# Optimization experiments

Measured on AMD Instinct MI355X. Metric: run time of the kernel, lower is better.

## Reference

```python
import jax, jax.numpy as jnp
import numpy as np

B, L, N, H = 512, 50, 16, 128
NUM_USERS = NUM_ITEMS = 100000


def setup_inputs() -> dict:
    key = jax.random.key(0)
    ks = jax.random.split(key, 20)
    s = lambda i, shape: jax.random.normal(ks[i], shape, dtype=jnp.float32) * 0.05
    return {
        "user_ids": jax.random.randint(ks[0], (B,), 0, NUM_USERS),
        "item_ids": jax.random.randint(ks[1], (B,), 0, NUM_ITEMS),
        "history": jax.random.randint(ks[2], (B, L), 0, NUM_ITEMS),
        "neighbor_emb": jax.random.normal(ks[3], (B, L, N, H), dtype=jnp.float32),
        "user_table": s(4, (NUM_USERS, H)),
        "item_table": s(5, (NUM_ITEMS, H)),
        "Wa": s(6, (2 * H, 96)), "ba": jnp.zeros((96,), jnp.float32),
        "W1": s(7, (96, 48)), "b1": jnp.zeros((48,), jnp.float32),
        "W2": s(8, (48, 16)), "b2": jnp.zeros((16,), jnp.float32),
        "W3": s(9, (16, 1)), "b3": jnp.zeros((1,), jnp.float32),
        # 4 heads of Linear(H, H//4) concatenated on the output dim == one [H, H] GEMM
        "Wmh": s(10, (H, H)), "bmh": jnp.zeros((H,), jnp.float32),
        "Wfc1": s(11, (2 * H, H)), "bfc1": jnp.zeros((H,), jnp.float32),
        "Wout": s(12, (H, 1)), "bout": jnp.zeros((1,), jnp.float32),
    }


def reference(user_ids, item_ids, history, neighbor_emb,
              user_table, item_table, Wa, ba, W1, b1, W2, b2, W3, b3,
              Wmh, bmh, Wfc1, bfc1, Wout, bout):
    user_emb = user_table[user_ids]                      # [B, H]
    item_emb = item_table[item_ids]                      # computed but unused (as in original)
    hist_emb = item_table[history]                       # [B, L, H]

    # concat(history broadcast over neighbors, neighbor_emb) -> [B, L, N, 2H]
    hist_b = jnp.broadcast_to(hist_emb[:, :, None, :], (B, L, N, H))
    att_in = jnp.concatenate([hist_b, neighbor_emb], axis=-1)

    scores = jax.nn.relu(att_in @ Wa + ba)               # [B, L, N, 96]
    h1 = jax.nn.relu(scores @ W1 + b1)                   # [B, L, N, 48]
    h2 = jax.nn.relu(h1 @ W2 + b2)                       # [B, L, N, 16]
    logits = (h2 @ W3 + b3)[..., 0]                      # [B, L, N]
    attn = jax.nn.softmax(logits, axis=-1)               # softmax over neighbor dim

    agg = jnp.einsum('bln,blnh->blh', attn, neighbor_emb)  # [B, L, H]
    mh = agg @ Wmh + bmh                                 # fused multihead projections
    pooled = mh.mean(axis=1)                             # [B, H]

    comb = jnp.concatenate([user_emb, pooled], axis=-1)  # [B, 2H]
    hidden = jax.nn.relu(comb @ Wfc1 + bfc1)             # dropout is identity in eval
    out = jax.nn.sigmoid(hidden @ Wout + bout)[:, 0]     # [B]
    return out
```

## Files before the change

### kernel.cpp

```cpp
#include <hip/hip_runtime.h>

constexpr int B  = 512, L = 50, N = 16, H = 128;
constexpr int C1 = 96, C2 = 48, C3 = 16;

typedef __bf16   bf16x8 __attribute__((ext_vector_type(8)));
typedef float    f32x4  __attribute__((ext_vector_type(4)));
typedef unsigned u32x4  __attribute__((ext_vector_type(4)));

__device__ __forceinline__ bf16x8 cvt8(float4 a, float4 b) {
  bf16x8 r;
  r[0] = (__bf16)a.x; r[1] = (__bf16)a.y; r[2] = (__bf16)a.z; r[3] = (__bf16)a.w;
  r[4] = (__bf16)b.x; r[5] = (__bf16)b.y; r[6] = (__bf16)b.z; r[7] = (__bf16)b.w;
  return r;
}
__device__ __forceinline__ float bf16lo(unsigned u) { return __uint_as_float(u << 16); }
__device__ __forceinline__ float bf16hi(unsigned u) { return __uint_as_float(u & 0xffff0000u); }
__device__ __forceinline__ unsigned pkbf(float lo, float hi) {
  unsigned r;
  asm("v_cvt_pk_bf16_f32 %0, %1, %2" : "=v"(r) : "v"(lo), "v"(hi));
  return r;
}

__global__ __launch_bounds__(256, 2) void fused_kernel(
    const int*   __restrict__ user_ids,
    const int*   __restrict__ history,
    const float* __restrict__ neighbor_emb,
    const float* __restrict__ user_table,
    const float* __restrict__ item_table,
    const float* __restrict__ Wa,  const float* __restrict__ ba,
    const float* __restrict__ W1,  const float* __restrict__ b1,
    const float* __restrict__ W2,  const float* __restrict__ b2,
    const float* __restrict__ W3,
    const float* __restrict__ Wmh,  const float* __restrict__ bmh,
    const float* __restrict__ Wfc1, const float* __restrict__ bfc1,
    const float* __restrict__ Wout, const float* __restrict__ bout,
    float* __restrict__ out)
{
  __shared__ __align__(16) __bf16 sWa[48 * 64 * 8];
  __shared__ __align__(16) __bf16 sW1[9 * 64 * 8];
  __shared__ __align__(16) __bf16 sW2f[2 * 64 * 8];
  __shared__ __align__(16) __bf16 sHS[4][16 * C1];
  __shared__ __align__(16) float sB1[48];
  __shared__ __align__(16) float sB2[16];
  __shared__ __align__(16) float sW3v[16];
  __shared__ float sRed[4][128];
  __shared__ float sAgg2[128];
  __shared__ float sComb[2 * H];
  __shared__ float sP[4];

  const int tid  = threadIdx.x;
  const int wave = tid >> 6;
  const int lane = tid & 63;
  const int g    = lane >> 4;
  const int c    = lane & 15;

  for (int e = tid; e < 48 * 64; e += 256) {
    int lv = e & 63, frag = e >> 6;
    int s = frag & 7, t = frag >> 3;
    int k0 = s * 32 + ((lv >> 4) << 3);
    int cc = t * 16 + (lv & 15);
    bf16x8 v;
    #pragma unroll
    for (int j = 0; j < 8; ++j) v[j] = (__bf16)Wa[(k0 + j) * C1 + cc];
    *(bf16x8*)&sWa[e * 8] = v;
  }
  for (int e = tid; e < 9 * 64; e += 256) {
    int lv = e & 63, frag = e >> 6;
    int s = frag % 3, t = frag / 3;
    int k0 = s * 32 + ((lv >> 4) << 3);
    int cc = t * 16 + (lv & 15);
    bf16x8 v;
    #pragma unroll
    for (int j = 0; j < 8; ++j) v[j] = (__bf16)W1[(k0 + j) * C2 + cc];
    *(bf16x8*)&sW1[e * 8] = v;
  }
  for (int e = tid; e < 2 * 64; e += 256) {
    int lv = e & 63, s = e >> 6;
    bf16x8 v;
    #pragma unroll
    for (int j = 0; j < 8; ++j) {
      int k = s * 32 + ((lv >> 4) << 3) + j;
      v[j] = (k < C2) ? (__bf16)W2[k * C3 + (lv & 15)] : (__bf16)0.f;
    }
    *(bf16x8*)&sW2f[e * 8] = v;
  }
  if (tid < 48) sB1[tid] = b1[tid];
  if (tid < 16) { sB2[tid] = b2[tid]; sW3v[tid] = W3[tid]; }

  __syncthreads();

  const int bb = blockIdx.x;
  const int wl = wave;
  __bf16* HS = sHS[wave];
  const int nIter = (L - wl + 3) / 4;

  {
    float ba_r[6];
    #pragma unroll
    for (int t = 0; t < 6; ++t) ba_r[t] = ba[t * 16 + c];
    int li  = wl + 4 * c;
    int idx = (li < L) ? history[bb * L + li] : history[bb * L];
    const float* hr = item_table + (size_t)idx * H;
    f32x4 acch[6];
    #pragma unroll
    for (int t = 0; t < 6; ++t) acch[t] = (f32x4){0.f, 0.f, 0.f, 0.f};
    #pragma unroll
    for (int s = 0; s < 4; ++s) {
      const float* p = hr + s * 32 + g * 8;
      bf16x8 a = cvt8(*(const float4*)p, *(const float4*)(p + 4));
      #pragma unroll
      for (int t = 0; t < 6; ++t)
        acch[t] = __builtin_amdgcn_mfma_f32_16x16x32_bf16(
            a, *(const bf16x8*)&sWa[((t * 8 + s) * 64 + lane) * 8], acch[t], 0, 0, 0);
    }
    #pragma unroll
    for (int t = 0; t < 6; ++t)
      #pragma unroll
      for (int r = 0; r < 4; ++r)
        HS[(4 * g + r) * C1 + t * 16 + c] = (__bf16)(acch[t][r] + ba_r[t]);
  }

  const float* nb0 = neighbor_emb + (size_t)(bb * L + wl) * (N * H) + c * H + g * 8;
  const size_t TS = (size_t)4 * N * H;
  float4 nf[8];
  #pragma unroll
  for (int s = 0; s < 4; ++s) {
    nf[2 * s]     = *(const float4*)(nb0 + s * 32);
    nf[2 * s + 1] = *(const float4*)(nb0 + s * 32 + 4);
  }
  float aggp[32];
  #pragma unroll
  for (int i = 0; i < 32; ++i) aggp[i] = 0.f;

  const int  src_lo = ((g & 1) << 5) | c;
  const int  src_hi = src_lo + 16;
  const bool gh     = (g >> 1) & 1;

  for (int it = 0; it < nIter; ++it) {
    bf16x8 aA[4];
    #pragma unroll
    for (int s = 0; s < 4; ++s) aA[s] = cvt8(nf[2 * s], nf[2 * s + 1]);
    if (it + 1 < nIter) {
      const float* p = nb0 + (size_t)(it + 1) * TS;
      #pragma unroll
      for (int s = 0; s < 4; ++s) {
        nf[2 * s]     = *(const float4*)(p + s * 32);
        nf[2 * s + 1] = *(const float4*)(p + s * 32 + 4);
      }
    }

    unsigned lo_ = 0;
    asm volatile("" : "+v"(lo_));
    const f32x4 b1v0 = *(const f32x4*)&sB1[ 0 + 4 * g + lo_];
    const f32x4 b1v1 = *(const f32x4*)&sB1[16 + 4 * g + lo_];
    const f32x4 b1v2 = *(const f32x4*)&sB1[32 + 4 * g + lo_];
    const f32x4 b2v  = *(const f32x4*)&sB2[4 * g + lo_];
    const f32x4 w3v  = *(const f32x4*)&sW3v[4 * g + lo_];
    const bf16x8 w2f0 = *(const bf16x8*)&sW2f[(0 * 64 + lane) * 8 + lo_ * 8];
    const bf16x8 w2f1 = *(const bf16x8*)&sW2f[(1 * 64 + lane) * 8 + lo_ * 8];

    f32x4 acc[6];
    #pragma unroll
    for (int t = 0; t < 6; ++t) {
      uint2 hw = *(const uint2*)&HS[it * C1 + 16 * t + 4 * g];
      acc[t][0] = bf16lo(hw.x); acc[t][1] = bf16hi(hw.x);
      acc[t][2] = bf16lo(hw.y); acc[t][3] = bf16hi(hw.y);
    }
    #pragma unroll
    for (int s = 0; s < 4; ++s)
      #pragma unroll
      for (int t = 0; t < 6; ++t)
        acc[t] = __builtin_amdgcn_mfma_f32_16x16x32_bf16(
            *(const bf16x8*)&sWa[((t * 8 + 4 + s) * 64 + lane) * 8], aA[s],
            acc[t], 0, 0, 0);
    unsigned pku[6][2];
    #pragma unroll
    for (int t = 0; t < 6; ++t) {
      pku[t][0] = pkbf(fmaxf(acc[t][0], 0.f), fmaxf(acc[t][1], 0.f));
      pku[t][1] = pkbf(fmaxf(acc[t][2], 0.f), fmaxf(acc[t][3], 0.f));
    }

    f32x4 acc2[3] = {b1v0, b1v1, b1v2};
    #pragma unroll
    for (int s = 0; s < 3; ++s) {
      unsigned a0 = __shfl((int)pku[2 * s][0], src_lo);
      unsigned a1 = __shfl((int)pku[2 * s][1], src_lo);
      unsigned a2 = __shfl((int)pku[2 * s][0], src_hi);
      unsigned a3 = __shfl((int)pku[2 * s][1], src_hi);
      unsigned d0 = __shfl((int)pku[2 * s + 1][0], src_lo);
      unsigned d1 = __shfl((int)pku[2 * s + 1][1], src_lo);
      unsigned d2 = __shfl((int)pku[2 * s + 1][0], src_hi);
      unsigned d3 = __shfl((int)pku[2 * s + 1][1], src_hi);
      u32x4 wv = {gh ? d0 : a0, gh ? d1 : a1, gh ? d2 : a2, gh ? d3 : a3};
      bf16x8 bf2 = __builtin_bit_cast(bf16x8, wv);
      #pragma unroll
      for (int t2 = 0; t2 < 3; ++t2)
        acc2[t2] = __builtin_amdgcn_mfma_f32_16x16x32_bf16(
            *(const bf16x8*)&sW1[((t2 * 3 + s) * 64 + lane) * 8], bf2,
            acc2[t2], 0, 0, 0);
    }
    unsigned pk2[3][2];
    #pragma unroll
    for (int t2 = 0; t2 < 3; ++t2) {
      pk2[t2][0] = pkbf(fmaxf(acc2[t2][0], 0.f), fmaxf(acc2[t2][1], 0.f));
      pk2[t2][1] = pkbf(fmaxf(acc2[t2][2], 0.f), fmaxf(acc2[t2][3], 0.f));
    }

    f32x4 acc3 = b2v;
    {
      unsigned a0 = __shfl((int)pk2[0][0], src_lo);
      unsigned a1 = __shfl((int)pk2[0][1], src_lo);
      unsigned a2 = __shfl((int)pk2[0][0], src_hi);
      unsigned a3 = __shfl((int)pk2[0][1], src_hi);
      unsigned d0 = __shfl((int)pk2[1][0], src_lo);
      unsigned d1 = __shfl((int)pk2[1][1], src_lo);
      unsigned d2 = __shfl((int)pk2[1][0], src_hi);
      unsigned d3 = __shfl((int)pk2[1][1], src_hi);
      u32x4 wv = {gh ? d0 : a0, gh ? d1 : a1, gh ? d2 : a2, gh ? d3 : a3};
      acc3 = __builtin_amdgcn_mfma_f32_16x16x32_bf16(
          w2f0, __builtin_bit_cast(bf16x8, wv), acc3, 0, 0, 0);
      unsigned e0 = __shfl((int)pk2[2][0], src_lo);
      unsigned e1 = __shfl((int)pk2[2][1], src_lo);
      unsigned e2 = __shfl((int)pk2[2][0], src_hi);
      unsigned e3 = __shfl((int)pk2[2][1], src_hi);
      u32x4 wv2 = {gh ? 0u : e0, gh ? 0u : e1, gh ? 0u : e2, gh ? 0u : e3};
      acc3 = __builtin_amdgcn_mfma_f32_16x16x32_bf16(
          w2f1, __builtin_bit_cast(bf16x8, wv2), acc3, 0, 0, 0);
    }

    float lg = 0.f;
    #pragma unroll
    for (int r = 0; r < 4; ++r) lg = fmaf(fmaxf(acc3[r], 0.f), w3v[r], lg);
    lg += __shfl_xor(lg, 16);
    lg += __shfl_xor(lg, 32);
    float e = __expf(lg);
    float se = e;
    se += __shfl_xor(se, 1);
    se += __shfl_xor(se, 2);
    se += __shfl_xor(se, 4);
    se += __shfl_xor(se, 8);
    const float w = e / se;

    #pragma unroll
    for (int s = 0; s < 4; ++s) {
      u32x4 au = __builtin_bit_cast(u32x4, aA[s]);
      #pragma unroll
      for (int q = 0; q < 4; ++q) {
        unsigned u = au[q];
        aggp[s * 8 + 2 * q]     = fmaf(w, bf16lo(u), aggp[s * 8 + 2 * q]);
        aggp[s * 8 + 2 * q + 1] = fmaf(w, bf16hi(u), aggp[s * 8 + 2 * q + 1]);
      }
    }
  }

  #pragma unroll
  for (int off = 1; off < 16; off <<= 1)
    #pragma unroll
    for (int i = 0; i < 32; ++i) aggp[i] += __shfl_xor(aggp[i], off);
  if (c == 0) {
    #pragma unroll
    for (int s = 0; s < 4; ++s) {
      float4 v0 = {aggp[8 * s + 0], aggp[8 * s + 1], aggp[8 * s + 2], aggp[8 * s + 3]};
      float4 v1 = {aggp[8 * s + 4], aggp[8 * s + 5], aggp[8 * s + 6], aggp[8 * s + 7]};
      *(float4*)&sRed[wave][32 * s + 8 * g]     = v0;
      *(float4*)&sRed[wave][32 * s + 8 * g + 4] = v1;
    }
  }
  __syncthreads();

  if (tid < 128) {
    float s = 0.f;
    #pragma unroll
    for (int w = 0; w < 4; ++w) s += sRed[w][tid];
    sAgg2[tid] = s * (1.0f / L);
    sComb[tid] = user_table[(size_t)user_ids[bb] * H + tid];
  }
  __syncthreads();
  if (tid < 128) {
    float p = bmh[tid];
    #pragma unroll 8
    for (int k = 0; k < H; ++k) p = fmaf(sAgg2[k], Wmh[k * H + tid], p);
    sComb[H + tid] = p;
  }
  __syncthreads();
  if (tid < 128) {
    float hd = bfc1[tid];
    #pragma unroll 8
    for (int k = 0; k < 2 * H; ++k) hd = fmaf(sComb[k], Wfc1[k * H + tid], hd);
    hd = fmaxf(hd, 0.f);
    float partial = hd * Wout[tid];
    #pragma unroll
    for (int off = 32; off > 0; off >>= 1) partial += __shfl_down(partial, off);
    if (lane == 0) sP[wave] = partial;
  }
  __syncthreads();
  if (tid == 0)
    out[bb] = 1.f / (1.f + __expf(-(sP[0] + sP[1] + bout[0])));
}

extern "C" void kernel_launch(void* const* d_in, const int* in_sizes, int n_in,
                              void* d_out, int out_size, void* d_ws, size_t ws_size,
                              hipStream_t stream) {
  const int*   user_ids     = (const int*)  d_in[0];
  const int*   history      = (const int*)  d_in[2];
  const float* neighbor_emb = (const float*)d_in[3];
  const float* user_table   = (const float*)d_in[4];
  const float* item_table   = (const float*)d_in[5];
  const float* Wa   = (const float*)d_in[6];
  const float* ba   = (const float*)d_in[7];
  const float* W1   = (const float*)d_in[8];
  const float* b1   = (const float*)d_in[9];
  const float* W2   = (const float*)d_in[10];
  const float* b2   = (const float*)d_in[11];
  const float* W3   = (const float*)d_in[12];
  const float* Wmh  = (const float*)d_in[14];
  const float* bmh  = (const float*)d_in[15];
  const float* Wfc1 = (const float*)d_in[16];
  const float* bfc1 = (const float*)d_in[17];
  const float* Wout = (const float*)d_in[18];
  const float* bout = (const float*)d_in[19];

  float* out = (float*)d_out;

  hipLaunchKernelGGL(fused_kernel, dim3(B), dim3(256), 0, stream,
                     user_ids, history, neighbor_emb, user_table, item_table,
                     Wa, ba, W1, b1, W2, b2, W3,
                     Wmh, bmh, Wfc1, bfc1, Wout, bout, out);
}
```

Baseline: 59.52 us.

## Split attention across two blocks per batch row and move MLP head to separate kernel

The fused kernel is split in two. The attention kernel now launches two blocks per batch row, each handling half the history positions, and writes partial aggregates to workspace. A second small kernel combines the halves and runs the Wmh/Wfc1/output head. Wa is staged in LDS one half at a time (history half, then neighbor half) to cut shared memory, which may allow higher occupancy. The cost is an extra launch, a workspace round trip, and Wa being re-staged once per block.

```diff
diff --git a/kernel.cpp b/kernel.cpp
--- a/kernel.cpp
+++ b/kernel.cpp
@@ -21,32 +21,24 @@
   return r;
 }
 
-__global__ __launch_bounds__(256, 2) void fused_kernel(
-    const int*   __restrict__ user_ids,
+__global__ __launch_bounds__(256, 2) void attn_kernel(
     const int*   __restrict__ history,
     const float* __restrict__ neighbor_emb,
-    const float* __restrict__ user_table,
     const float* __restrict__ item_table,
     const float* __restrict__ Wa,  const float* __restrict__ ba,
     const float* __restrict__ W1,  const float* __restrict__ b1,
     const float* __restrict__ W2,  const float* __restrict__ b2,
     const float* __restrict__ W3,
-    const float* __restrict__ Wmh,  const float* __restrict__ bmh,
-    const float* __restrict__ Wfc1, const float* __restrict__ bfc1,
-    const float* __restrict__ Wout, const float* __restrict__ bout,
-    float* __restrict__ out)
+    float* __restrict__ ws)
 {
-  __shared__ __align__(16) __bf16 sWa[48 * 64 * 8];
+  __shared__ __align__(16) __bf16 sWa[24 * 64 * 8];
   __shared__ __align__(16) __bf16 sW1[9 * 64 * 8];
   __shared__ __align__(16) __bf16 sW2f[2 * 64 * 8];
-  __shared__ __align__(16) __bf16 sHS[4][16 * C1];
+  __shared__ __align__(16) __bf16 sHS[4][8 * C1];
   __shared__ __align__(16) float sB1[48];
   __shared__ __align__(16) float sB2[16];
   __shared__ __align__(16) float sW3v[16];
   __shared__ float sRed[4][128];
-  __shared__ float sAgg2[128];
-  __shared__ float sComb[2 * H];
-  __shared__ float sP[4];
 
   const int tid  = threadIdx.x;
   const int wave = tid >> 6;
@@ -54,9 +46,13 @@
   const int g    = lane >> 4;
   const int c    = lane & 15;
 
-  for (int e = tid; e < 48 * 64; e += 256) {
+  const int bb     = blockIdx.x >> 1;
+  const int half   = blockIdx.x & 1;
+  const int stream = half * 4 + wave;
+
+  for (int e = tid; e < 24 * 64; e += 256) {
     int lv = e & 63, frag = e >> 6;
-    int s = frag & 7, t = frag >> 3;
+    int s = frag & 3, t = frag >> 2;
     int k0 = s * 32 + ((lv >> 4) << 3);
     int cc = t * 16 + (lv & 15);
     bf16x8 v;
@@ -89,16 +85,14 @@
 
   __syncthreads();
 
-  const int bb = blockIdx.x;
-  const int wl = wave;
   __bf16* HS = sHS[wave];
-  const int nIter = (L - wl + 3) / 4;
+  const int nIter = (L - stream + 7) / 8;
 
   {
     float ba_r[6];
     #pragma unroll
     for (int t = 0; t < 6; ++t) ba_r[t] = ba[t * 16 + c];
-    int li  = wl + 4 * c;
+    int li  = stream + 8 * c;
     int idx = (li < L) ? history[bb * L + li] : history[bb * L];
     const float* hr = item_table + (size_t)idx * H;
     f32x4 acch[6];
@@ -111,17 +105,33 @@
       #pragma unroll
       for (int t = 0; t < 6; ++t)
         acch[t] = __builtin_amdgcn_mfma_f32_16x16x32_bf16(
-            a, *(const bf16x8*)&sWa[((t * 8 + s) * 64 + lane) * 8], acch[t], 0, 0, 0);
-    }
-    #pragma unroll
-    for (int t = 0; t < 6; ++t)
-      #pragma unroll
-      for (int r = 0; r < 4; ++r)
-        HS[(4 * g + r) * C1 + t * 16 + c] = (__bf16)(acch[t][r] + ba_r[t]);
-  }
-
-  const float* nb0 = neighbor_emb + (size_t)(bb * L + wl) * (N * H) + c * H + g * 8;
-  const size_t TS = (size_t)4 * N * H;
+            a, *(const bf16x8*)&sWa[((t * 4 + s) * 64 + lane) * 8], acch[t], 0, 0, 0);
+    }
+    if (g < 2) {
+      #pragma unroll
+      for (int t = 0; t < 6; ++t)
+        #pragma unroll
+        for (int r = 0; r < 4; ++r)
+          HS[(4 * g + r) * C1 + t * 16 + c] = (__bf16)(acch[t][r] + ba_r[t]);
+    }
+  }
+
+  __syncthreads();
+
+  for (int e = tid; e < 24 * 64; e += 256) {
+    int lv = e & 63, frag = e >> 6;
+    int s = frag & 3, t = frag >> 2;
+    int k0 = 128 + s * 32 + ((lv >> 4) << 3);
+    int cc = t * 16 + (lv & 15);
+    bf16x8 v;
+    #pragma unroll
+    for (int j = 0; j < 8; ++j) v[j] = (__bf16)Wa[(k0 + j) * C1 + cc];
+    *(bf16x8*)&sWa[e * 8] = v;
+  }
+  __syncthreads();
+
+  const float* nb0 = neighbor_emb + (size_t)(bb * L + stream) * (N * H) + c * H + g * 8;
+  const size_t TS = (size_t)8 * N * H;
   float4 nf[8];
   #pragma unroll
   for (int s = 0; s < 4; ++s) {
@@ -171,7 +181,7 @@
       #pragma unroll
       for (int t = 0; t < 6; ++t)
         acc[t] = __builtin_amdgcn_mfma_f32_16x16x32_bf16(
-            *(const bf16x8*)&sWa[((t * 8 + 4 + s) * 64 + lane) * 8], aA[s],
+            *(const bf16x8*)&sWa[((t * 4 + s) * 64 + lane) * 8], aA[s],
             acc[t], 0, 0, 0);
     unsigned pku[6][2];
     #pragma unroll
@@ -272,30 +282,50 @@
     float s = 0.f;
     #pragma unroll
     for (int w = 0; w < 4; ++w) s += sRed[w][tid];
-    sAgg2[tid] = s * (1.0f / L);
-    sComb[tid] = user_table[(size_t)user_ids[bb] * H + tid];
-  }
-  __syncthreads();
-  if (tid < 128) {
-    float p = bmh[tid];
-    #pragma unroll 8
-    for (int k = 0; k < H; ++k) p = fmaf(sAgg2[k], Wmh[k * H + tid], p);
-    sComb[H + tid] = p;
-  }
-  __syncthreads();
-  if (tid < 128) {
-    float hd = bfc1[tid];
-    #pragma unroll 8
-    for (int k = 0; k < 2 * H; ++k) hd = fmaf(sComb[k], Wfc1[k * H + tid], hd);
-    hd = fmaxf(hd, 0.f);
-    float partial = hd * Wout[tid];
-    #pragma unroll
-    for (int off = 32; off > 0; off >>= 1) partial += __shfl_down(partial, off);
-    if (lane == 0) sP[wave] = partial;
-  }
-  __syncthreads();
-  if (tid == 0)
-    out[bb] = 1.f / (1.f + __expf(-(sP[0] + sP[1] + bout[0])));
+    ws[(size_t)blockIdx.x * 128 + tid] = s;
+  }
+}
+
+__global__ __launch_bounds__(128) void head_kernel(
+    const int*   __restrict__ user_ids,
+    const float* __restrict__ user_table,
+    const float* __restrict__ ws,
+    const float* __restrict__ Wmh,  const float* __restrict__ bmh,
+    const float* __restrict__ Wfc1, const float* __restrict__ bfc1,
+    const float* __restrict__ Wout, const float* __restrict__ bout,
+    float* __restrict__ out)
+{
+  __shared__ float sComb[2 * H];
+  __shared__ float sAgg[H];
+  __shared__ float sRed[2];
+  const int t = threadIdx.x, b = blockIdx.x;
+
+  int uid = user_ids[b];
+  sComb[t] = user_table[(size_t)uid * H + t];
+  sAgg[t]  = (ws[(size_t)(2 * b) * 128 + t] + ws[(size_t)(2 * b + 1) * 128 + t])
+             * (1.0f / L);
+  __syncthreads();
+
+  float p = bmh[t];
+  #pragma unroll 8
+  for (int k = 0; k < H; ++k) p = fmaf(sAgg[k], Wmh[k * H + t], p);
+  sComb[H + t] = p;
+  __syncthreads();
+
+  float hd = bfc1[t];
+  #pragma unroll 8
+  for (int k = 0; k < 2 * H; ++k) hd = fmaf(sComb[k], Wfc1[k * H + t], hd);
+  hd = fmaxf(hd, 0.f);
+
+  float v = hd * Wout[t];
+  #pragma unroll
+  for (int off = 32; off > 0; off >>= 1) v += __shfl_down(v, off);
+  if ((t & 63) == 0) sRed[t >> 6] = v;
+  __syncthreads();
+  if (t == 0) {
+    float s = sRed[0] + sRed[1] + bout[0];
+    out[b] = 1.f / (1.f + __expf(-s));
+  }
 }
 
 extern "C" void kernel_launch(void* const* d_in, const int* in_sizes, int n_in,
@@ -320,10 +350,13 @@
   const float* Wout = (const float*)d_in[18];
   const float* bout = (const float*)d_in[19];
 
+  float* ws  = (float*)d_ws;
   float* out = (float*)d_out;
 
-  hipLaunchKernelGGL(fused_kernel, dim3(B), dim3(256), 0, stream,
-                     user_ids, history, neighbor_emb, user_table, item_table,
-                     Wa, ba, W1, b1, W2, b2, W3,
+  hipLaunchKernelGGL(attn_kernel, dim3(B * 2), dim3(256), 0, stream,
+                     history, neighbor_emb, item_table,
+                     Wa, ba, W1, b1, W2, b2, W3, ws);
+  hipLaunchKernelGGL(head_kernel, dim3(B), dim3(128), 0, stream,
+                     user_ids, user_table, ws,
                      Wmh, bmh, Wfc1, bfc1, Wout, bout, out);
 }
```

Result: slower. 77.51 us (+30.2%).
